# Optimization experiments

Measured on AMD Instinct MI355X. Metric: run time of the kernel, lower is better.

The kernel has to match this reference:

```python
import jax, jax.numpy as jnp
import numpy as np

DIM = 1024
GROUP = 16
N_LIN = 18   # 6 blocks * 3 quantized linears
N_LN = 5
RANK = 32
BATCH = 32768


def _dequant(q, s):
    # q: [DIM, DIM] int values in [0,16); s: [DIM*DIM/GROUP] per-group scales
    w = (q.reshape(-1, GROUP).astype(jnp.float32) - 8.0) * s[:, None]
    return w.reshape(DIM, DIM)


def _qlora_linear(x, q, s, b, la, lb):
    # x: [N, DIM]; la: [RANK, DIM]; lb: [DIM, RANK]
    w = _dequant(q, s)
    base = x @ w.T + b
    lora = (x @ la.T) @ lb.T
    return base + lora


def _layernorm(x, g, b):
    m = jnp.mean(x, axis=-1, keepdims=True)
    v = jnp.var(x, axis=-1, keepdims=True)
    return (x - m) / jnp.sqrt(v + 1e-5) * g + b


def setup_inputs() -> dict:
    key = jax.random.key(0)
    ks = jax.random.split(key, 8)
    x = jax.random.normal(ks[0], (BATCH, DIM), dtype=jnp.float32)
    wq = jax.random.randint(ks[1], (N_LIN, DIM, DIM), 0, 16, dtype=jnp.int32)
    scales = jax.random.uniform(ks[2], (N_LIN, DIM * DIM // GROUP), dtype=jnp.float32) * 0.02 + 1e-3
    bias = jax.random.normal(ks[3], (N_LIN, DIM), dtype=jnp.float32) * 0.02
    lora_a = jax.random.normal(ks[4], (N_LIN, RANK, DIM), dtype=jnp.float32) * 0.05
    lora_b = jax.random.normal(ks[5], (N_LIN, DIM, RANK), dtype=jnp.float32) * 0.05
    gamma = jnp.ones((N_LN, DIM), dtype=jnp.float32)
    beta = jnp.zeros((N_LN, DIM), dtype=jnp.float32)
    return {"x": x, "wq": wq, "scales": scales, "bias": bias,
            "lora_a": lora_a, "lora_b": lora_b, "gamma": gamma, "beta": beta}


def reference(x, wq, scales, bias, lora_a, lora_b, gamma, beta):
    h = x.astype(jnp.float32)
    li = 0
    for blk in range(6):
        r = h
        for j in range(3):
            h = _qlora_linear(h, wq[li], scales[li], bias[li], lora_a[li], lora_b[li])
            li += 1
            if j < 2:
                h = jax.nn.relu(h)
        h = h + r
        if blk < 5:
            h = _layernorm(h, gamma[blk], beta[blk])
    return h
```

## Files before the change

kernel.cpp:

```cpp
#include <hip/hip_runtime.h>

typedef unsigned int u32;
typedef unsigned short u16;
typedef _Float16 f16;
typedef f16 f16x8 __attribute__((ext_vector_type(8)));
typedef float f32x4 __attribute__((ext_vector_type(4)));
typedef u16 u16x8 __attribute__((ext_vector_type(8)));

#define DIM 1024
#define BATCH 32768
#define RANK 32
#define NLIN 18

__device__ __forceinline__ u16 f2h(float f) {
    f16 h = (f16)f;
    return *(u16*)&h;
}
__device__ __forceinline__ float h2f(u16 u) {
    f16 h;
    *(u16*)&h = u;
    return (float)h;
}

__device__ __forceinline__ void gload16(const u16* g, u16* l) {
    __builtin_amdgcn_global_load_lds((__attribute__((address_space(1))) const void*)g,
                                     (__attribute__((address_space(3))) void*)l,
                                     16, 0, 0);
}

#define ASM_BAR()    asm volatile("s_barrier" ::: "memory")
#define ASM_VM0()    asm volatile("s_waitcnt vmcnt(0)" ::: "memory")
#define ASM_VM8()    asm volatile("s_waitcnt vmcnt(8)" ::: "memory")
#define ASM_LGKM0()  asm volatile("s_waitcnt lgkmcnt(0)" ::: "memory")

__global__ __launch_bounds__(256) void build_weff(
    const int* __restrict__ wq, const float* __restrict__ scales,
    const float* __restrict__ la, const float* __restrict__ lb,
    u16* __restrict__ weff)
{
    int rb = blockIdx.x;
    int li = blockIdx.y;
    int tid = threadIdx.x;
    int row0 = rb * 16;
    __shared__ float lb_s[16][RANK];
    __shared__ float la_s[RANK][256];
    for (int idx = tid; idx < 16 * RANK; idx += 256) {
        int o = idx >> 5, r = idx & 31;
        lb_s[o][r] = lb[((size_t)li * DIM + row0 + o) * RANK + r];
    }
    const int* wqL = wq + (size_t)li * DIM * DIM;
    const float* sL = scales + (size_t)li * (DIM * DIM / 16);
    u16* wout = weff + (size_t)li * DIM * DIM;
    for (int kc = 0; kc < DIM; kc += 256) {
        __syncthreads();
        #pragma unroll
        for (int j = 0; j < 32; ++j) {
            int idx = j * 256 + tid;
            int r = idx >> 8, c = idx & 255;
            la_s[r][c] = la[((size_t)li * RANK + r) * DIM + kc + c];
        }
        __syncthreads();
        int k = kc + tid;
        for (int o = 0; o < 16; ++o) {
            int og = row0 + o;
            float acc = ((float)wqL[og * DIM + k] - 8.0f) * sL[(og << 6) + (k >> 4)];
            #pragma unroll
            for (int r = 0; r < RANK; ++r)
                acc += lb_s[o][r] * la_s[r][tid];
            wout[og * DIM + k] = f2h(acc);
        }
    }
}

__global__ __launch_bounds__(256) void xcast(const float* __restrict__ x, u16* __restrict__ o) {
    size_t i = ((size_t)blockIdx.x * 256 + threadIdx.x) * 8;
    float4 a = *(const float4*)(x + i);
    float4 b = *(const float4*)(x + i + 4);
    u16x8 v;
    v[0] = f2h(a.x); v[1] = f2h(a.y); v[2] = f2h(a.z); v[3] = f2h(a.w);
    v[4] = f2h(b.x); v[5] = f2h(b.y); v[6] = f2h(b.z); v[7] = f2h(b.w);
    *(u16x8*)(o + i) = v;
}

template<int EPI>
__global__ __launch_bounds__(512, 2) void gemm256(
    const u16* __restrict__ X, const u16* __restrict__ W,
    const float* __restrict__ bias, const u16* __restrict__ res,
    void* __restrict__ outp)
{
    __shared__ __align__(16) u16 As[2][256 * 64];
    __shared__ __align__(16) u16 Bs[2][256 * 64];
    const int tid = threadIdx.x;
    const int bid = blockIdx.x;
    const int wg = (bid & 7) * 64 + (bid >> 3);
    const int bm = wg >> 2;
    const int bn = wg & 3;
    const int wid = tid >> 6;
    const int lane = tid & 63;
    const int wm = wid >> 2;
    const int wn = wid & 3;

    const int c1 = tid, c2 = tid + 512;
    const int r1 = c1 >> 3, r2 = c2 >> 3;
    const int l1 = ((c1 & 7) ^ (r1 & 7)) * 8;
    const int l2 = ((c2 & 7) ^ (r2 & 7)) * 8;
    const u16* gA0a = X + (size_t)(bm * 256 +       r1) * DIM + l1;
    const u16* gA0b = X + (size_t)(bm * 256 +       r2) * DIM + l2;
    const u16* gA1a = X + (size_t)(bm * 256 + 128 + r1) * DIM + l1;
    const u16* gA1b = X + (size_t)(bm * 256 + 128 + r2) * DIM + l2;
    const u16* gB0a = W + (size_t)(bn * 256 +       r1) * DIM + l1;
    const u16* gB0b = W + (size_t)(bn * 256 +       r2) * DIM + l2;
    const u16* gB1a = W + (size_t)(bn * 256 + 128 + r1) * DIM + l1;
    const u16* gB1b = W + (size_t)(bn * 256 + 128 + r2) * DIM + l2;
    const int d1 = c1 * 8, d2 = c2 * 8;

    const int kg = lane >> 4;
    const int sw = lane & 7;
    const int ch0 = ((0 * 4 + kg) ^ sw) * 8;
    const int ch1 = ((1 * 4 + kg) ^ sw) * 8;
    const int aoff = (wm * 128 + (lane & 15)) * 64;
    const int boff = (wn * 64 + (lane & 15)) * 64;

    f32x4 acc[8][4];
    #pragma unroll
    for (int i = 0; i < 8; ++i)
        #pragma unroll
        for (int j = 0; j < 4; ++j)
            acc[i][j] = (f32x4){0.f, 0.f, 0.f, 0.f};
    f16x8 af[4][2], bf[4][2];

    gload16(gA0a, &As[0][d1]);        gload16(gA0b, &As[0][d2]);
    gload16(gA1a, &As[0][8192 + d1]); gload16(gA1b, &As[0][8192 + d2]);
    gload16(gB0a, &Bs[0][d1]);        gload16(gB0b, &Bs[0][d2]);
    gload16(gB1a, &Bs[0][8192 + d1]); gload16(gB1b, &Bs[0][8192 + d2]);
    gload16(gA0a + 64, &As[1][d1]);        gload16(gA0b + 64, &As[1][d2]);
    gload16(gA1a + 64, &As[1][8192 + d1]); gload16(gA1b + 64, &As[1][8192 + d2]);
    gload16(gB0a + 64, &Bs[1][d1]);        gload16(gB0b + 64, &Bs[1][d2]);
    gload16(gB1a + 64, &Bs[1][8192 + d1]); gload16(gB1b + 64, &Bs[1][8192 + d2]);

    #define RD_A(MH) { \
        _Pragma("unroll") \
        for (int fm = 0; fm < 4; ++fm) { \
            af[fm][0] = *(const f16x8*)&Ab[aoff + ((MH)*64 + fm*16)*64 + ch0]; \
            af[fm][1] = *(const f16x8*)&Ab[aoff + ((MH)*64 + fm*16)*64 + ch1]; \
        } }
    #define RD_B(NH) { \
        _Pragma("unroll") \
        for (int fn = 0; fn < 2; ++fn) { \
            bf[(NH)*2+fn][0] = *(const f16x8*)&Bb[boff + (((NH)*2+fn)*16)*64 + ch0]; \
            bf[(NH)*2+fn][1] = *(const f16x8*)&Bb[boff + (((NH)*2+fn)*16)*64 + ch1]; \
        } }
    #define QUAD(MH, NH) { \
        __builtin_amdgcn_s_setprio(1); \
        _Pragma("unroll") \
        for (int ks = 0; ks < 2; ++ks) \
            _Pragma("unroll") \
            for (int fm = 0; fm < 4; ++fm) \
                _Pragma("unroll") \
                for (int fn = 0; fn < 2; ++fn) \
                    acc[(MH)*4+fm][(NH)*2+fn] = __builtin_amdgcn_mfma_f32_16x16x32_f16( \
                        af[fm][ks], bf[(NH)*2+fn][ks], acc[(MH)*4+fm][(NH)*2+fn], 0, 0, 0); \
        __builtin_amdgcn_s_setprio(0); }

    #pragma unroll 1
    for (int t = 0; t < 16; ++t) {
        const int p = t & 1;
        const bool pre = (t < 14);
        const int ko2 = (t + 2) * 64;
        const u16* Ab = &As[p][0];
        const u16* Bb = &Bs[p][0];
        u16* Aw = &As[p][0];
        u16* Bw = &Bs[p][0];
        if (pre) ASM_VM8(); else ASM_VM0();
        ASM_BAR();
        RD_A(0); RD_B(0);
        QUAD(0, 0);
        ASM_BAR();
        RD_B(1);
        QUAD(0, 1);
        ASM_BAR();
        if (pre) {
            gload16(gB0a + ko2, &Bw[d1]);        gload16(gB0b + ko2, &Bw[d2]);
            gload16(gB1a + ko2, &Bw[8192 + d1]); gload16(gB1b + ko2, &Bw[8192 + d2]);
        }
        RD_A(1);
        QUAD(1, 0);
        ASM_BAR();
        if (pre) {
            gload16(gA0a + ko2, &Aw[d1]);        gload16(gA0b + ko2, &Aw[d2]);
            gload16(gA1a + ko2, &Aw[8192 + d1]); gload16(gA1b + ko2, &Aw[8192 + d2]);
        }
        QUAD(1, 1);
    }

    ASM_LGKM0();
    ASM_BAR();
    float* blk = (float*)&As[0][0] + wid * 1088;
    const int mrow = bm * 256 + wm * 128;
    const int ncol = bn * 256 + wn * 64 + (lane & 7) * 8;
    float4 bv0 = *(const float4*)&bias[ncol];
    float4 bv1 = *(const float4*)&bias[ncol + 4];
    #pragma unroll
    for (int fm = 0; fm < 8; ++fm) {
        __builtin_amdgcn_sched_barrier(0);
        #pragma unroll
        for (int fn = 0; fn < 4; ++fn)
            #pragma unroll
            for (int reg = 0; reg < 4; ++reg)
                blk[((lane >> 4) * 4 + reg) * 68 + (lane & 15) + fn * 16] = acc[fm][fn][reg];
        ASM_LGKM0();
        __builtin_amdgcn_sched_barrier(0);
        #pragma unroll
        for (int pass = 0; pass < 2; ++pass) {
            const float* rp = &blk[(pass * 8 + (lane >> 3)) * 68 + (lane & 7) * 8];
            float4 v0 = *(const float4*)rp;
            float4 v1 = *(const float4*)(rp + 4);
            v0.x += bv0.x; v0.y += bv0.y; v0.z += bv0.z; v0.w += bv0.w;
            v1.x += bv1.x; v1.y += bv1.y; v1.z += bv1.z; v1.w += bv1.w;
            const int m = mrow + fm * 16 + pass * 8 + (lane >> 3);
            const size_t gi = (size_t)m * DIM + ncol;
            if (EPI == 0) {
                u16x8 o;
                o[0] = f2h(fmaxf(v0.x, 0.f)); o[1] = f2h(fmaxf(v0.y, 0.f));
                o[2] = f2h(fmaxf(v0.z, 0.f)); o[3] = f2h(fmaxf(v0.w, 0.f));
                o[4] = f2h(fmaxf(v1.x, 0.f)); o[5] = f2h(fmaxf(v1.y, 0.f));
                o[6] = f2h(fmaxf(v1.z, 0.f)); o[7] = f2h(fmaxf(v1.w, 0.f));
                *(u16x8*)((u16*)outp + gi) = o;
            } else {
                u16x8 rv = *(const u16x8*)(res + gi);
                v0.x += h2f(rv[0]); v0.y += h2f(rv[1]); v0.z += h2f(rv[2]); v0.w += h2f(rv[3]);
                v1.x += h2f(rv[4]); v1.y += h2f(rv[5]); v1.z += h2f(rv[6]); v1.w += h2f(rv[7]);
                if (EPI == 1) {
                    u16x8 o;
                    o[0] = f2h(v0.x); o[1] = f2h(v0.y); o[2] = f2h(v0.z); o[3] = f2h(v0.w);
                    o[4] = f2h(v1.x); o[5] = f2h(v1.y); o[6] = f2h(v1.z); o[7] = f2h(v1.w);
                    *(u16x8*)((u16*)outp + gi) = o;
                } else {
                    *(float4*)((float*)outp + gi) = v0;
                    *(float4*)((float*)outp + gi + 4) = v1;
                }
            }
        }
        ASM_LGKM0();
    }
    #undef RD_A
    #undef RD_B
    #undef QUAD
}

__global__ __launch_bounds__(256) void ln_k(const u16* __restrict__ in,
    const float* __restrict__ g, const float* __restrict__ b, u16* __restrict__ out)
{
    int row = blockIdx.x * 4 + (threadIdx.x >> 6);
    int lane = threadIdx.x & 63;
    const u16* rp = in + (size_t)row * DIM;
    u16x8 v0 = *(const u16x8*)(rp + lane * 8);
    u16x8 v1 = *(const u16x8*)(rp + 512 + lane * 8);
    float f[16];
    #pragma unroll
    for (int j = 0; j < 8; ++j) { f[j] = h2f(v0[j]); f[8 + j] = h2f(v1[j]); }
    float s = 0.f, sq = 0.f;
    #pragma unroll
    for (int j = 0; j < 16; ++j) { s += f[j]; sq += f[j] * f[j]; }
    #pragma unroll
    for (int m = 1; m < 64; m <<= 1) { s += __shfl_xor(s, m); sq += __shfl_xor(sq, m); }
    float mean = s * (1.0f / 1024.0f);
    float var = sq * (1.0f / 1024.0f) - mean * mean;
    float rstd = 1.0f / sqrtf(var + 1e-5f);
    u16x8 o0, o1;
    #pragma unroll
    for (int j = 0; j < 8; ++j) {
        int c0 = lane * 8 + j, c1 = 512 + lane * 8 + j;
        o0[j] = f2h((f[j] - mean) * rstd * g[c0] + b[c0]);
        o1[j] = f2h((f[8 + j] - mean) * rstd * g[c1] + b[c1]);
    }
    u16* op = out + (size_t)row * DIM;
    *(u16x8*)(op + lane * 8) = o0;
    *(u16x8*)(op + 512 + lane * 8) = o1;
}

extern "C" void kernel_launch(void* const* d_in, const int* in_sizes, int n_in,
                              void* d_out, int out_size, void* d_ws, size_t ws_size,
                              hipStream_t stream) {
    const float* x      = (const float*)d_in[0];
    const int*   wq     = (const int*)d_in[1];
    const float* scales = (const float*)d_in[2];
    const float* bias   = (const float*)d_in[3];
    const float* la     = (const float*)d_in[4];
    const float* lb     = (const float*)d_in[5];
    const float* gamma  = (const float*)d_in[6];
    const float* beta   = (const float*)d_in[7];

    char* ws = (char*)d_ws;
    u16* Weff = (u16*)ws;
    u16* actA = (u16*)(ws + (size_t)NLIN * DIM * DIM * 2);
    u16* actB = actA + (size_t)BATCH * DIM;
    u16* dob  = (u16*)d_out;
    float* dof = (float*)d_out;

    build_weff<<<dim3(64, 18), 256, 0, stream>>>(wq, scales, la, lb, Weff);
    xcast<<<(BATCH * DIM) / 2048, 256, 0, stream>>>(x, actA);

    int li = 0;
    for (int blk = 0; blk < 6; ++blk) {
        const u16* w0 = Weff + (size_t)(li + 0) * DIM * DIM;
        const u16* w1 = Weff + (size_t)(li + 1) * DIM * DIM;
        const u16* w2 = Weff + (size_t)(li + 2) * DIM * DIM;
        const float* b0 = bias + (li + 0) * DIM;
        const float* b1 = bias + (li + 1) * DIM;
        const float* b2 = bias + (li + 2) * DIM;
        if (blk < 5) {
            gemm256<0><<<512, 512, 0, stream>>>(actA, w0, b0, nullptr, actB);
            gemm256<0><<<512, 512, 0, stream>>>(actB, w1, b1, nullptr, dob);
            gemm256<1><<<512, 512, 0, stream>>>(dob,  w2, b2, actA, actB);
            ln_k<<<BATCH / 4, 256, 0, stream>>>(actB, gamma + blk * DIM, beta + blk * DIM, actA);
        } else {
            gemm256<0><<<512, 512, 0, stream>>>(actA, w0, b0, nullptr, dob);
            gemm256<0><<<512, 512, 0, stream>>>(dob,  w1, b1, nullptr, actB);
            gemm256<2><<<512, 512, 0, stream>>>(actB, w2, b2, actA, (void*)dof);
        }
        li += 3;
    }
}
```

Measured before the change: 1.498 ms.

## Double-buffer GEMM register fragments and prefetch next tile's LDS reads during MFMAs

Restructures the GEMM main loop into an unrolled pair of tiles that ping-pong between two sets of A/B register fragments. The next tile's LDS fragment reads are issued before the current tile's last MFMA quads. Fine-grained lgkmcnt and vmcnt waits replace the coarse per-tile waits, and the prologue reorders its global loads so B arrives before A. The aim is to hide LDS read latency and barrier stalls behind matrix-core work, at the cost of more registers and delicate wait-count correctness.

```diff
diff --git a/kernel.cpp b/kernel.cpp
--- a/kernel.cpp
+++ b/kernel.cpp
@@ -28,10 +28,12 @@
                                      16, 0, 0);
 }
 
-#define ASM_BAR()    asm volatile("s_barrier" ::: "memory")
+#define BAR()        __builtin_amdgcn_s_barrier()
 #define ASM_VM0()    asm volatile("s_waitcnt vmcnt(0)" ::: "memory")
-#define ASM_VM8()    asm volatile("s_waitcnt vmcnt(8)" ::: "memory")
-#define ASM_LGKM0()  asm volatile("s_waitcnt lgkmcnt(0)" ::: "memory")
+#define ASM_VM4()    asm volatile("s_waitcnt vmcnt(4)" ::: "memory")
+#define ASM_LG0()    asm volatile("s_waitcnt lgkmcnt(0)" ::: "memory")
+#define ASM_LG4()    asm volatile("s_waitcnt lgkmcnt(4)" ::: "memory")
+#define ASM_LG8()    asm volatile("s_waitcnt lgkmcnt(8)" ::: "memory")
 
 __global__ __launch_bounds__(256) void build_weff(
     const int* __restrict__ wq, const float* __restrict__ scales,
@@ -127,30 +129,31 @@
         #pragma unroll
         for (int j = 0; j < 4; ++j)
             acc[i][j] = (f32x4){0.f, 0.f, 0.f, 0.f};
-    f16x8 af[4][2], bf[4][2];
+    f16x8 afH0[4][2], afH1[4][2];
+    f16x8 bf0[4][2], bf1[4][2];
 
     gload16(gA0a, &As[0][d1]);        gload16(gA0b, &As[0][d2]);
     gload16(gA1a, &As[0][8192 + d1]); gload16(gA1b, &As[0][8192 + d2]);
     gload16(gB0a, &Bs[0][d1]);        gload16(gB0b, &Bs[0][d2]);
     gload16(gB1a, &Bs[0][8192 + d1]); gload16(gB1b, &Bs[0][8192 + d2]);
+    gload16(gB0a + 64, &Bs[1][d1]);        gload16(gB0b + 64, &Bs[1][d2]);
+    gload16(gB1a + 64, &Bs[1][8192 + d1]); gload16(gB1b + 64, &Bs[1][8192 + d2]);
     gload16(gA0a + 64, &As[1][d1]);        gload16(gA0b + 64, &As[1][d2]);
     gload16(gA1a + 64, &As[1][8192 + d1]); gload16(gA1b + 64, &As[1][8192 + d2]);
-    gload16(gB0a + 64, &Bs[1][d1]);        gload16(gB0b + 64, &Bs[1][d2]);
-    gload16(gB1a + 64, &Bs[1][8192 + d1]); gload16(gB1b + 64, &Bs[1][8192 + d2]);
-
-    #define RD_A(MH) { \
+
+    #define RD_A(AF, MH, BUF) { \
         _Pragma("unroll") \
         for (int fm = 0; fm < 4; ++fm) { \
-            af[fm][0] = *(const f16x8*)&Ab[aoff + ((MH)*64 + fm*16)*64 + ch0]; \
-            af[fm][1] = *(const f16x8*)&Ab[aoff + ((MH)*64 + fm*16)*64 + ch1]; \
+            AF[fm][0] = *(const f16x8*)&(BUF)[aoff + ((MH)*64 + fm*16)*64 + ch0]; \
+            AF[fm][1] = *(const f16x8*)&(BUF)[aoff + ((MH)*64 + fm*16)*64 + ch1]; \
         } }
-    #define RD_B(NH) { \
+    #define RD_B(BF, NH, BUF) { \
         _Pragma("unroll") \
         for (int fn = 0; fn < 2; ++fn) { \
-            bf[(NH)*2+fn][0] = *(const f16x8*)&Bb[boff + (((NH)*2+fn)*16)*64 + ch0]; \
-            bf[(NH)*2+fn][1] = *(const f16x8*)&Bb[boff + (((NH)*2+fn)*16)*64 + ch1]; \
+            BF[(NH)*2+fn][0] = *(const f16x8*)&(BUF)[boff + (((NH)*2+fn)*16)*64 + ch0]; \
+            BF[(NH)*2+fn][1] = *(const f16x8*)&(BUF)[boff + (((NH)*2+fn)*16)*64 + ch1]; \
         } }
-    #define QUAD(MH, NH) { \
+    #define QUAD(MH, NH, AF, BF) { \
         __builtin_amdgcn_s_setprio(1); \
         _Pragma("unroll") \
         for (int ks = 0; ks < 2; ++ks) \
@@ -159,42 +162,57 @@
                 _Pragma("unroll") \
                 for (int fn = 0; fn < 2; ++fn) \
                     acc[(MH)*4+fm][(NH)*2+fn] = __builtin_amdgcn_mfma_f32_16x16x32_f16( \
-                        af[fm][ks], bf[(NH)*2+fn][ks], acc[(MH)*4+fm][(NH)*2+fn], 0, 0, 0); \
+                        AF[fm][ks], BF[(NH)*2+fn][ks], acc[(MH)*4+fm][(NH)*2+fn], 0, 0, 0); \
         __builtin_amdgcn_s_setprio(0); }
 
+    asm volatile("s_waitcnt vmcnt(8)" ::: "memory");
+    BAR();
+    RD_A(afH0, 0, (&As[0][0]));
+    RD_B(bf0, 0, (&Bs[0][0]));
+
+    #define TILE(T, PT, BFC, BFN) { \
+         \
+        RD_B(BFC, 1, (&Bs[PT][0])); \
+        ASM_LG4(); \
+        QUAD(0, 0, afH0, BFC); \
+        BAR(); \
+         \
+        RD_A(afH1, 1, (&As[PT][0])); \
+        ASM_LG8(); \
+        QUAD(0, 1, afH0, BFC); \
+        if ((T) < 15) ASM_VM4(); \
+        BAR(); \
+         \
+        if ((T) < 14) { \
+            const int ko2 = ((T) + 2) * 64; \
+            gload16(gB0a + ko2, &Bs[PT][d1]);        gload16(gB0b + ko2, &Bs[PT][d2]); \
+            gload16(gB1a + ko2, &Bs[PT][8192 + d1]); gload16(gB1b + ko2, &Bs[PT][8192 + d2]); \
+        } \
+        if ((T) < 15) { RD_B(BFN, 0, (&Bs[(PT)^1][0])); ASM_LG4(); } else { ASM_LG0(); } \
+        QUAD(1, 0, afH1, BFC); \
+        if ((T) < 14) ASM_VM4(); else if ((T) == 14) ASM_VM0(); \
+        BAR(); \
+         \
+        if ((T) < 14) { \
+            const int ko2 = ((T) + 2) * 64; \
+            gload16(gA0a + ko2, &As[PT][d1]);        gload16(gA0b + ko2, &As[PT][d2]); \
+            gload16(gA1a + ko2, &As[PT][8192 + d1]); gload16(gA1b + ko2, &As[PT][8192 + d2]); \
+        } \
+        if ((T) < 15) { RD_A(afH0, 0, (&As[(PT)^1][0])); ASM_LG8(); } else { ASM_LG0(); } \
+        QUAD(1, 1, afH1, BFC); \
+        BAR(); \
+    }
+
     #pragma unroll 1
-    for (int t = 0; t < 16; ++t) {
-        const int p = t & 1;
-        const bool pre = (t < 14);
-        const int ko2 = (t + 2) * 64;
-        const u16* Ab = &As[p][0];
-        const u16* Bb = &Bs[p][0];
-        u16* Aw = &As[p][0];
-        u16* Bw = &Bs[p][0];
-        if (pre) ASM_VM8(); else ASM_VM0();
-        ASM_BAR();
-        RD_A(0); RD_B(0);
-        QUAD(0, 0);
-        ASM_BAR();
-        RD_B(1);
-        QUAD(0, 1);
-        ASM_BAR();
-        if (pre) {
-            gload16(gB0a + ko2, &Bw[d1]);        gload16(gB0b + ko2, &Bw[d2]);
-            gload16(gB1a + ko2, &Bw[8192 + d1]); gload16(gB1b + ko2, &Bw[8192 + d2]);
-        }
-        RD_A(1);
-        QUAD(1, 0);
-        ASM_BAR();
-        if (pre) {
-            gload16(gA0a + ko2, &Aw[d1]);        gload16(gA0b + ko2, &Aw[d2]);
-            gload16(gA1a + ko2, &Aw[8192 + d1]); gload16(gA1b + ko2, &Aw[8192 + d2]);
-        }
-        QUAD(1, 1);
-    }
-
-    ASM_LGKM0();
-    ASM_BAR();
+    for (int tp = 0; tp < 8; ++tp) {
+        const int T0 = tp * 2;
+        const int T1 = T0 + 1;
+        TILE(T0, 0, bf0, bf1);
+        TILE(T1, 1, bf1, bf0);
+    }
+
+    ASM_LG0();
+    BAR();
     float* blk = (float*)&As[0][0] + wid * 1088;
     const int mrow = bm * 256 + wm * 128;
     const int ncol = bn * 256 + wn * 64 + (lane & 7) * 8;
@@ -208,7 +226,7 @@
             #pragma unroll
             for (int reg = 0; reg < 4; ++reg)
                 blk[((lane >> 4) * 4 + reg) * 68 + (lane & 15) + fn * 16] = acc[fm][fn][reg];
-        ASM_LGKM0();
+        ASM_LG0();
         __builtin_amdgcn_sched_barrier(0);
         #pragma unroll
         for (int pass = 0; pass < 2; ++pass) {
@@ -241,11 +259,12 @@
                 }
             }
         }
-        ASM_LGKM0();
+        ASM_LG0();
     }
     #undef RD_A
     #undef RD_B
     #undef QUAD
+    #undef TILE
 }
 
 __global__ __launch_bounds__(256) void ln_k(const u16* __restrict__ in,
```

Result: slower. 3.395 ms (+126.6%).

## Software-pipeline LDS fragment reads across half-iterations in GEMM main loop

Applied to the files above, without the earlier changes.

Restructures the double-buffered GEMM main loop so the LDS fragment reads for the next half-tile (and the next k-step's buffer) are issued before the MFMAs that consume the current ones. It cuts barriers per iteration from four to two, loads all B fragments at once, and reorders the prologue so B arrives before A, with vmcnt waits adjusted to match. The aim is to hide LDS read latency behind MFMA work. In exchange it holds more fragment registers live and depends on delicate wait and barrier ordering.

```diff
diff --git a/kernel.cpp b/kernel.cpp
--- a/kernel.cpp
+++ b/kernel.cpp
@@ -28,10 +28,11 @@
                                      16, 0, 0);
 }
 
-#define ASM_BAR()    asm volatile("s_barrier" ::: "memory")
+#define BAR()        __builtin_amdgcn_s_barrier()
+#define SB0()        __builtin_amdgcn_sched_barrier(0)
 #define ASM_VM0()    asm volatile("s_waitcnt vmcnt(0)" ::: "memory")
-#define ASM_VM8()    asm volatile("s_waitcnt vmcnt(8)" ::: "memory")
-#define ASM_LGKM0()  asm volatile("s_waitcnt lgkmcnt(0)" ::: "memory")
+#define ASM_VM4()    asm volatile("s_waitcnt vmcnt(4)" ::: "memory")
+#define ASM_LG0()    asm volatile("s_waitcnt lgkmcnt(0)" ::: "memory")
 
 __global__ __launch_bounds__(256) void build_weff(
     const int* __restrict__ wq, const float* __restrict__ scales,
@@ -127,28 +128,29 @@
         #pragma unroll
         for (int j = 0; j < 4; ++j)
             acc[i][j] = (f32x4){0.f, 0.f, 0.f, 0.f};
-    f16x8 af[4][2], bf[4][2];
+    f16x8 af[4][2];
+    f16x8 bf[4][2];
 
     gload16(gA0a, &As[0][d1]);        gload16(gA0b, &As[0][d2]);
     gload16(gA1a, &As[0][8192 + d1]); gload16(gA1b, &As[0][8192 + d2]);
     gload16(gB0a, &Bs[0][d1]);        gload16(gB0b, &Bs[0][d2]);
     gload16(gB1a, &Bs[0][8192 + d1]); gload16(gB1b, &Bs[0][8192 + d2]);
+    gload16(gB0a + 64, &Bs[1][d1]);        gload16(gB0b + 64, &Bs[1][d2]);
+    gload16(gB1a + 64, &Bs[1][8192 + d1]); gload16(gB1b + 64, &Bs[1][8192 + d2]);
     gload16(gA0a + 64, &As[1][d1]);        gload16(gA0b + 64, &As[1][d2]);
     gload16(gA1a + 64, &As[1][8192 + d1]); gload16(gA1b + 64, &As[1][8192 + d2]);
-    gload16(gB0a + 64, &Bs[1][d1]);        gload16(gB0b + 64, &Bs[1][d2]);
-    gload16(gB1a + 64, &Bs[1][8192 + d1]); gload16(gB1b + 64, &Bs[1][8192 + d2]);
-
-    #define RD_A(MH) { \
+
+    #define RD_A(MH, BUF) { \
         _Pragma("unroll") \
         for (int fm = 0; fm < 4; ++fm) { \
-            af[fm][0] = *(const f16x8*)&Ab[aoff + ((MH)*64 + fm*16)*64 + ch0]; \
-            af[fm][1] = *(const f16x8*)&Ab[aoff + ((MH)*64 + fm*16)*64 + ch1]; \
+            af[fm][0] = *(const f16x8*)&(BUF)[aoff + ((MH)*64 + fm*16)*64 + ch0]; \
+            af[fm][1] = *(const f16x8*)&(BUF)[aoff + ((MH)*64 + fm*16)*64 + ch1]; \
         } }
-    #define RD_B(NH) { \
+    #define RD_B(BUF) { \
         _Pragma("unroll") \
-        for (int fn = 0; fn < 2; ++fn) { \
-            bf[(NH)*2+fn][0] = *(const f16x8*)&Bb[boff + (((NH)*2+fn)*16)*64 + ch0]; \
-            bf[(NH)*2+fn][1] = *(const f16x8*)&Bb[boff + (((NH)*2+fn)*16)*64 + ch1]; \
+        for (int fn = 0; fn < 4; ++fn) { \
+            bf[fn][0] = *(const f16x8*)&(BUF)[boff + (fn*16)*64 + ch0]; \
+            bf[fn][1] = *(const f16x8*)&(BUF)[boff + (fn*16)*64 + ch1]; \
         } }
     #define QUAD(MH, NH) { \
         __builtin_amdgcn_s_setprio(1); \
@@ -162,39 +164,46 @@
                         af[fm][ks], bf[(NH)*2+fn][ks], acc[(MH)*4+fm][(NH)*2+fn], 0, 0, 0); \
         __builtin_amdgcn_s_setprio(0); }
 
+    asm volatile("s_waitcnt vmcnt(8)" ::: "memory");
+    BAR();
+    RD_A(0, (&As[0][0]));
+    RD_B((&Bs[0][0]));
+
     #pragma unroll 1
     for (int t = 0; t < 16; ++t) {
         const int p = t & 1;
-        const bool pre = (t < 14);
+        const u16* Ap = &As[p][0];
+        u16* Awr = &As[p][0];
+        u16* Bwr = &Bs[p][0];
+        const u16* An = &As[p ^ 1][0];
+        const u16* Bn = &Bs[p ^ 1][0];
         const int ko2 = (t + 2) * 64;
-        const u16* Ab = &As[p][0];
-        const u16* Bb = &Bs[p][0];
-        u16* Aw = &As[p][0];
-        u16* Bw = &Bs[p][0];
-        if (pre) ASM_VM8(); else ASM_VM0();
-        ASM_BAR();
-        RD_A(0); RD_B(0);
-        QUAD(0, 0);
-        ASM_BAR();
-        RD_B(1);
-        QUAD(0, 1);
-        ASM_BAR();
-        if (pre) {
-            gload16(gB0a + ko2, &Bw[d1]);        gload16(gB0b + ko2, &Bw[d2]);
-            gload16(gB1a + ko2, &Bw[8192 + d1]); gload16(gB1b + ko2, &Bw[8192 + d2]);
-        }
-        RD_A(1);
-        QUAD(1, 0);
-        ASM_BAR();
-        if (pre) {
-            gload16(gA0a + ko2, &Aw[d1]);        gload16(gA0b + ko2, &Aw[d2]);
-            gload16(gA1a + ko2, &Aw[8192 + d1]); gload16(gA1b + ko2, &Aw[8192 + d2]);
-        }
-        QUAD(1, 1);
-    }
-
-    ASM_LGKM0();
-    ASM_BAR();
+        BAR();
+        ASM_LG0(); SB0();
+        QUAD(0, 0); QUAD(0, 1);
+        RD_A(1, Ap);
+        if (t <= 13) {
+            gload16(gB0a + ko2, &Bwr[d1]);        gload16(gB0b + ko2, &Bwr[d2]);
+            gload16(gB1a + ko2, &Bwr[8192 + d1]); gload16(gB1b + ko2, &Bwr[8192 + d2]);
+        }
+        SB0();
+        if (t <= 13) ASM_VM4(); else if (t == 14) ASM_VM0();
+        BAR();
+        ASM_LG0(); SB0();
+        QUAD(1, 0); QUAD(1, 1);
+        if (t <= 14) {
+            RD_A(0, An);
+            RD_B(Bn);
+        }
+        if (t <= 13) {
+            gload16(gA0a + ko2, &Awr[d1]);        gload16(gA0b + ko2, &Awr[d2]);
+            gload16(gA1a + ko2, &Awr[8192 + d1]); gload16(gA1b + ko2, &Awr[8192 + d2]);
+        }
+        SB0();
+    }
+
+    ASM_LG0();
+    BAR();
     float* blk = (float*)&As[0][0] + wid * 1088;
     const int mrow = bm * 256 + wm * 128;
     const int ncol = bn * 256 + wn * 64 + (lane & 7) * 8;
@@ -208,7 +217,7 @@
             #pragma unroll
             for (int reg = 0; reg < 4; ++reg)
                 blk[((lane >> 4) * 4 + reg) * 68 + (lane & 15) + fn * 16] = acc[fm][fn][reg];
-        ASM_LGKM0();
+        ASM_LG0();
         __builtin_amdgcn_sched_barrier(0);
         #pragma unroll
         for (int pass = 0; pass < 2; ++pass) {
@@ -241,7 +250,7 @@
                 }
             }
         }
-        ASM_LGKM0();
+        ASM_LG0();
     }
     #undef RD_A
     #undef RD_B
```

Result: faster. 1.421 ms (-5.2%).
